# Kernel optimization log

Measured on AMD Instinct MI355X. Metric: run time of the kernel, lower is better.

## Reference

```python
import jax, jax.numpy as jnp
import numpy as np

N, E, IN, H, O, ED = 20000, 100000, 167, 4, 256, 10
HID = H * O  # 1024
BN_EPS = 1e-5


def _bn(x, g, b):
    # BatchNorm1d in training mode: batch statistics over nodes
    mu = x.mean(0)
    var = x.var(0)
    return (x - mu) * jax.lax.rsqrt(var + BN_EPS) * g + b


def _gat(x, src, dst, ef, Wg, We, attn, at, cb, heads, out):
    # modified_GAT: multi-head attention with edge features + time scalar
    n = x.shape[0]
    h = (x @ Wg).reshape(n, heads, out)                 # [N,H,O]
    e = (ef[:, 1:] @ We).reshape(-1, heads, out)        # [E,H,O] edge-feature proj
    t = ef[:, 0]                                        # [E] time feature
    # node-level attention scores (avoids materializing [E,H,O] twice)
    s_src = jnp.einsum('nhd,hd->nh', h, attn[0])
    s_dst = jnp.einsum('nhd,hd->nh', h, attn[1])
    s_e = jnp.einsum('ehd,hd->eh', e, attn[2])
    logits = jax.nn.leaky_relu(s_src[src] + s_dst[dst] + s_e + t[:, None] * at, 0.2)  # [E,H]
    # attention normalization: softmax over incoming edges of each dst node
    m = jax.ops.segment_max(logits, dst, num_segments=n)
    m = jnp.where(jnp.isfinite(m), m, 0.0)
    p = jnp.exp(logits - m[dst])
    denom = jax.ops.segment_sum(p, dst, num_segments=n)
    w = p / (denom[dst] + 1e-16)                        # [E,H]
    msg = w[:, :, None] * (h[src] + e)                  # [E,H,O]
    agg = jax.ops.segment_sum(msg, dst, num_segments=n) # [N,H,O]
    return agg.reshape(n, heads * out) + cb


def setup_inputs() -> dict:
    key = jax.random.key(0)
    ks = iter(jax.random.split(key, 64))

    def nrm(shape, s):
        return jax.random.normal(next(ks), shape, dtype=jnp.float32) * np.float32(s)

    d = {}
    d['x'] = jax.random.normal(next(ks), (N, IN), dtype=jnp.float32)
    d['edge_index'] = jax.random.randint(next(ks), (2, E), 0, N)
    d['edge_attr'] = jax.random.uniform(next(ks), (E, ED + 2), dtype=jnp.float32)
    conv_dims = [(IN, H, O), (HID, H, O), (HID, 1, 2)]
    for i, (fin, hh, oo) in enumerate(conv_dims, 1):
        d[f'Wg{i}'] = nrm((fin, hh * oo), 1.0 / np.sqrt(fin))
        d[f'We{i}'] = nrm((ED, hh * oo), 1.0 / np.sqrt(ED))
        d[f'attn{i}'] = nrm((3, hh, oo), 0.1)
        d[f'at{i}'] = nrm((hh,), 0.1)
        d[f'cb{i}'] = jnp.zeros((hh * oo,), jnp.float32)
    lin_dims = [(IN, HID), (HID, HID), (HID, 2)]
    bn_dims = [IN, HID, HID]
    for i, (fin, fo) in enumerate(lin_dims, 1):
        d[f'lw{i}'] = nrm((fin, fo), 1.0 / np.sqrt(fin))
        d[f'lb{i}'] = jnp.zeros((fo,), jnp.float32)
        d[f'g{i}'] = jnp.ones((bn_dims[i - 1],), jnp.float32)
        d[f'b{i}'] = jnp.zeros((bn_dims[i - 1],), jnp.float32)
    return d


def reference(x, edge_index, edge_attr,
              Wg1, We1, attn1, at1, cb1, lw1, lb1, g1, b1,
              Wg2, We2, attn2, at2, cb2, lw2, lb2, g2, b2,
              Wg3, We3, attn3, at3, cb3, lw3, lb3, g3, b3):
    src, dst = edge_index[0], edge_index[1]
    ef = edge_attr[:, :-1]  # drop edge class column
    h = _bn(x, g1, b1)
    h = jax.nn.relu(h @ lw1 + lb1 + _gat(h, src, dst, ef, Wg1, We1, attn1, at1, cb1, H, O))
    h = _bn(h, g2, b2)
    h = jax.nn.relu(h @ lw2 + lb2 + _gat(h, src, dst, ef, Wg2, We2, attn2, at2, cb2, H, O))
    h = _bn(h, g3, b3)
    h = jax.nn.relu(h @ lw3 + lb3 + _gat(h, src, dst, ef, Wg3, We3, attn3, at3, cb3, 1, 2))
    return h
```

## Files before the change

### kernel.cpp

```cpp
#include <hip/hip_runtime.h>
#include <math.h>

#define NN 20000
#define EE 100000
#define FIN 167
#define KP1 192
#define HID 1024
#define OO 256
#define NB 8

typedef unsigned short u16;
typedef short bf16x8 __attribute__((ext_vector_type(8)));
typedef short s16x4  __attribute__((ext_vector_type(4)));
typedef float f32x4  __attribute__((ext_vector_type(4)));

__device__ __forceinline__ float bf(u16 u){ return __uint_as_float(((unsigned)u)<<16); }
__device__ __forceinline__ u16 fb(float v){
  unsigned u = __float_as_uint(v);
  return (u16)((u + 0x7FFFu + ((u>>16)&1u)) >> 16);
}
__device__ __forceinline__ float ldv(const float* p, long i){ return p[i]; }
__device__ __forceinline__ float ldv(const u16*   p, long i){ return bf(p[i]); }

__global__ void k_count(const int* __restrict__ ei, int* __restrict__ counts){
  int e = blockIdx.x*256 + threadIdx.x;
  if (e < EE) atomicAdd(&counts[ei[EE+e]], 1);
}

__global__ __launch_bounds__(256) void k_scanA(const int* __restrict__ counts,
                                               int* __restrict__ iptr, int* __restrict__ bsum){
  __shared__ int sd[256];
  int b = blockIdx.x, tid = threadIdx.x;
  int i = b*256 + tid;
  int v = (i<NN)? counts[i] : 0;
  sd[tid]=v; __syncthreads();
  for (int off=1; off<256; off<<=1){
    int t = (tid>=off)? sd[tid-off] : 0;
    __syncthreads();
    sd[tid] += t;
    __syncthreads();
  }
  if (i<NN) iptr[i] = sd[tid]-v;
  if (tid==255) bsum[b]=sd[255];
}
__global__ __launch_bounds__(128) void k_scanB(const int* __restrict__ bsum,
                                               int* __restrict__ boff, int* __restrict__ iptrN,
                                               int nb){
  __shared__ int sd[128];
  int tid=threadIdx.x;
  int v=(tid<nb)? bsum[tid]:0;
  sd[tid]=v; __syncthreads();
  for (int off=1; off<128; off<<=1){
    int t=(tid>=off)?sd[tid-off]:0;
    __syncthreads();
    sd[tid]+=t;
    __syncthreads();
  }
  if (tid<nb) boff[tid]=sd[tid]-v;
  if (tid==127) *iptrN = sd[127];
}
__global__ void k_scanC(const int* __restrict__ boff, int* __restrict__ iptr){
  int i = blockIdx.x*256+threadIdx.x;
  if (i<NN) iptr[i] += boff[blockIdx.x];
}

__global__ void k_fill(const int* __restrict__ ei, const int* __restrict__ iptr,
                       int* __restrict__ cursor, int* __restrict__ eid){
  int e = blockIdx.x*256 + threadIdx.x;
  if (e < EE){
    int d = ei[EE+e];
    int pos = atomicAdd(&cursor[d],1);
    eid[iptr[d]+pos] = e;
  }
}

template<typename T>
__global__ void k_bnstats(const T* __restrict__ X, float* __restrict__ sums, int F){
  int f = blockIdx.y*256 + threadIdx.x;
  if (f >= F) return;
  int r0 = blockIdx.x*100, r1 = r0+100;
  float s=0.f, s2=0.f;
  for (int r=r0;r<r1;r++){ float v = ldv(X,(long)r*F+f); s += v; s2 += v*v; }
  atomicAdd(&sums[f], s);
  atomicAdd(&sums[F+f], s2);
}

__global__ __launch_bounds__(256) void k_bnstats8(const u16* __restrict__ X, float* __restrict__ part){
  int tid = threadIdx.x;
  int f8 = (tid & 127)*8;
  int r0 = blockIdx.x*79, r1 = min(NN, r0+79);
  float s[8]={0,0,0,0,0,0,0,0}, s2[8]={0,0,0,0,0,0,0,0};
  for (int r=r0 + (tid>>7); r<r1; r+=2){
    bf16x8 v = *(const bf16x8*)(X + (long)r*HID + f8);
    #pragma unroll
    for (int j=0;j<8;j++){ float x=bf((u16)v[j]); s[j]+=x; s2[j]+=x*x; }
  }
  __shared__ float red[256][8];
  float* pb = part + (long)blockIdx.x*2048;
  #pragma unroll
  for (int j=0;j<8;j++) red[tid][j]=s[j];
  __syncthreads();
  if (tid<128){
    #pragma unroll
    for (int j=0;j<8;j++) pb[f8+j] = red[tid][j]+red[tid+128][j];
  }
  __syncthreads();
  #pragma unroll
  for (int j=0;j<8;j++) red[tid][j]=s2[j];
  __syncthreads();
  if (tid<128){
    #pragma unroll
    for (int j=0;j<8;j++) pb[1024+f8+j] = red[tid][j]+red[tid+128][j];
  }
}

__global__ __launch_bounds__(256) void k_pred(const float* __restrict__ part, float* __restrict__ sums){
  int idx = blockIdx.x*256 + threadIdx.x;
  float s = 0.f;
  #pragma unroll 8
  for (int b=0;b<256;b++) s += part[(long)b*2048 + idx];
  sums[idx] = s;
}

__global__ void k_bnfin(const float* __restrict__ sums, const float* __restrict__ g,
                        const float* __restrict__ b, float* __restrict__ scale,
                        float* __restrict__ shift, int F){
  int f = blockIdx.x*256 + threadIdx.x;
  if (f >= F) return;
  float mu  = sums[f]   * (1.f/NN);
  float var = sums[F+f] * (1.f/NN) - mu*mu;
  float sc  = rsqrtf(var + 1e-5f) * g[f];
  scale[f] = sc;
  shift[f] = b[f] - mu*sc;
}

__global__ __launch_bounds__(256) void k_foldT(const float* __restrict__ Wg, const float* __restrict__ Wl,
                        const float* __restrict__ scale,
                        u16* __restrict__ Wt, int K, int Kp){
  __shared__ float t[32][33];
  int k0 = blockIdx.x*32, c0 = blockIdx.y*32;
  int tx = threadIdx.x & 31, ty = threadIdx.x >> 5;
  bool second = (c0 >= HID);
  const float* W = second ? Wl : Wg;
  int cc0 = second ? c0 - HID : c0;
  #pragma unroll
  for (int i=0;i<4;i++){
    int k = k0 + ty + i*8;
    t[ty+i*8][tx] = (k < K) ? W[(long)k*HID + cc0 + tx] * scale[k] : 0.f;
  }
  __syncthreads();
  #pragma unroll
  for (int i=0;i<4;i++){
    int c = c0 + ty + i*8;
    Wt[(long)c*Kp + k0 + tx] = fb(t[tx][ty+i*8]);
  }
}

__global__ void k_cinit(const float* __restrict__ lb, float* __restrict__ cst){
  int c = blockIdx.x*256 + threadIdx.x;
  if (c < 2*HID) cst[c] = (c >= HID) ? lb[c-HID] : 0.f;
}

__global__ __launch_bounds__(256) void k_const(const float* __restrict__ Wg, const float* __restrict__ Wl,
                        const float* __restrict__ shift, float* __restrict__ cst, int K){
  int tx = threadIdx.x & 63, ty = threadIdx.x >> 6;
  int c = blockIdx.x*64 + tx;
  bool second = c >= HID;
  const float* W = second ? Wl : Wg;
  int cc = second ? c-HID : c;
  int k0 = blockIdx.y*128;
  int k1 = min(K, k0+128);
  float s = 0.f;
  for (int k=k0+ty; k<k1; k+=4) s += shift[k]*W[(long)k*HID+cc];
  __shared__ float red[256];
  red[threadIdx.x] = s;
  __syncthreads();
  if (ty == 0){
    float tot = red[tx] + red[tx+64] + red[tx+128] + red[tx+192];
    atomicAdd(&cst[c], tot);
  }
}

__global__ void k_cast(const float* __restrict__ x, u16* __restrict__ xb){
  long idx = (long)blockIdx.x*256 + threadIdx.x;
  if (idx >= (long)NN*KP1) return;
  int n = (int)(idx / KP1), k = (int)(idx % KP1);
  xb[idx] = (k<FIN)? fb(x[(long)n*FIN+k]) : (u16)0;
}

__global__ void k_we16(const float* __restrict__ We, u16* __restrict__ We16){
  int i = blockIdx.x*256 + threadIdx.x;
  if (i < 10*HID) We16[i] = fb(We[i]);
}

#define MF(a_,b_,c_) __builtin_amdgcn_mfma_f32_16x16x32_bf16(a_,b_,c_,0,0,0)
#define FENCE asm volatile("" ::: "memory")
#define BAR do { FENCE; __builtin_amdgcn_s_barrier(); FENCE; } while(0)

__global__ __launch_bounds__(512,2) void k_gemm(const u16* __restrict__ A, int K,
                     const u16* __restrict__ Wt, const float* __restrict__ cst,
                     u16* __restrict__ Chg, u16* __restrict__ Clin){
  __shared__ u16 lds[3][12288];
  int b = blockIdx.x;
  int wg = (b & 7)*158 + (b >> 3);
  int row0 = (wg >> 4)*256, col0 = (wg & 15)*128;
  int tid = threadIdx.x;
  int wave = tid >> 6, lane = tid & 63, quad = lane >> 4, lo = lane & 15;
  int wm = wave >> 1, wn = wave & 1;
  const u16* Apt[2];
  #pragma unroll
  for (int i=0;i<2;i++){
    int s = i*512 + tid, srow = s>>2;
    int gr = row0 + srow; if (gr >= NN) gr = NN-1;
    Apt[i] = A + (long)gr*K + (((s&3)^((srow>>1)&3))*8);
  }
  int brow = tid>>2;
  const u16* Bpt = Wt + (long)(col0 + brow)*K + ((((tid&3)^((brow>>1)&3)))*8);
  const char* ldsc = (const char*)&lds[0][0];
  int axor = (lo>>1) & 3;
  int aoff = (wm*64 + lo)*64 + ((quad^axor)*16);
  int boff = 16384 + (wn*64 + lo)*64 + ((quad^axor)*16);
  int NT = K >> 5;
  f32x4 acc[4][4] = {};
  {
    u16* d0 = (u16*)&lds[0][0];
    u16* d1 = (u16*)&lds[1][0];
    __builtin_amdgcn_global_load_lds(Apt[0],      d0 +         tid*8, 16, 0, 0);
    __builtin_amdgcn_global_load_lds(Apt[1],      d0 + 4096 +  tid*8, 16, 0, 0);
    __builtin_amdgcn_global_load_lds(Bpt,         d0 + 8192 +  tid*8, 16, 0, 0);
    __builtin_amdgcn_global_load_lds(Apt[0] + 32, d1 +         tid*8, 16, 0, 0);
    __builtin_amdgcn_global_load_lds(Apt[1] + 32, d1 + 4096 +  tid*8, 16, 0, 0);
    __builtin_amdgcn_global_load_lds(Bpt    + 32, d1 + 8192 +  tid*8, 16, 0, 0);
    asm volatile("s_waitcnt vmcnt(3)" ::: "memory");
    BAR;
  }
  int cb = 0;
  for (int t=0; t<NT; t++){
    const char* Lb = ldsc + cb*24576;
    bf16x8 af[4], bfr[4];
    #pragma unroll
    for (int i=0;i<4;i++) af[i]  = *(const bf16x8*)(Lb + aoff + i*1024);
    #pragma unroll
    for (int n=0;n<4;n++) bfr[n] = *(const bf16x8*)(Lb + boff + n*1024);
    int nx2 = (t+2 < NT);
    if (nx2){
      int sb = cb+2; if (sb>=3) sb-=3;
      u16* Sd = (u16*)&lds[0][0] + sb*12288;
      int ko = (t+2) << 5;
      __builtin_amdgcn_global_load_lds(Apt[0] + ko, Sd +         tid*8, 16, 0, 0);
      __builtin_amdgcn_global_load_lds(Apt[1] + ko, Sd + 4096 +  tid*8, 16, 0, 0);
      __builtin_amdgcn_global_load_lds(Bpt    + ko, Sd + 8192 +  tid*8, 16, 0, 0);
    }
    __builtin_amdgcn_s_setprio(1);
    #pragma unroll
    for (int i=0;i<4;i++)
      #pragma unroll
      for (int n=0;n<4;n++)
        acc[i][n] = MF(af[i], bfr[n], acc[i][n]);
    __builtin_amdgcn_s_setprio(0);
    if (t+1 < NT){
      if (nx2) asm volatile("s_waitcnt vmcnt(3)" ::: "memory");
      else     asm volatile("s_waitcnt vmcnt(0)" ::: "memory");
      BAR;
    }
    cb++; if (cb>=3) cb=0;
  }
  #pragma unroll
  for (int i=0;i<4;i++){
    #pragma unroll
    for (int n=0;n<4;n++){
      int col = col0 + wn*64 + n*16 + lo;
      float cs = cst[col];
      #pragma unroll
      for (int r=0;r<4;r++){
        int row = row0 + wm*64 + i*16 + quad*4 + r;
        if (row < NN){
          u16 o = fb(acc[i][n][r] + cs);
          if (col < HID) Chg[(long)row*HID + col] = o;
          else           Clin[(long)row*HID + col - HID] = o;
        }
      }
    }
  }
}
#undef MF
#undef BAR
#undef FENCE

__global__ __launch_bounds__(256) void k_sdot(const u16* __restrict__ hg, const float* __restrict__ attn,
                       float* __restrict__ ssrc, float* __restrict__ sdst){
  int unit = blockIdx.x*4 + (threadIdx.x >> 6);
  if (unit >= NN*4) return;
  int lane = threadIdx.x & 63;
  int n = unit >> 2, h = unit & 3;
  const u16* hp = hg + (long)n*HID + h*OO + lane*4;
  s16x4 v = *(const s16x4*)hp;
  float4 x0 = *(const float4*)(attn + h*OO + lane*4);
  float4 x1 = *(const float4*)(attn + HID + h*OO + lane*4);
  float f0 = bf((u16)v.x), f1 = bf((u16)v.y), f2 = bf((u16)v.z), f3 = bf((u16)v.w);
  float ss = f0*x0.x + f1*x0.y + f2*x0.z + f3*x0.w;
  float sd = f0*x1.x + f1*x1.y + f2*x1.z + f3*x1.w;
  #pragma unroll
  for (int off=32; off>0; off>>=1){
    ss += __shfl_down(ss, off);
    sd += __shfl_down(sd, off);
  }
  if (lane==0){ ssrc[unit]=ss; sdst[unit]=sd; }
}

__global__ void k_q(const float* __restrict__ We, const float* __restrict__ attn,
                    float* __restrict__ q){
  int t = threadIdx.x;
  if (t >= 40) return;
  int k = t >> 2, h = t & 3;
  float s = 0.f;
  for (int d=0; d<OO; d++) s += We[(long)k*HID + h*OO + d] * attn[2*HID + h*OO + d];
  q[k*4+h] = s;
}

__global__ void k_logits(const int* __restrict__ ei, const float* __restrict__ ea,
                         const float* __restrict__ q, const float* __restrict__ at,
                         const float* __restrict__ ssrc, const float* __restrict__ sdst,
                         float* __restrict__ L){
  int e = blockIdx.x*256 + threadIdx.x;
  if (e >= EE) return;
  int s = ei[e], dd = ei[EE+e];
  float4 a0 = *(const float4*)(ea + (long)e*12);
  float4 a1 = *(const float4*)(ea + (long)e*12 + 4);
  float4 a2 = *(const float4*)(ea + (long)e*12 + 8);
  float t = a0.x;
  float cc[10] = {a0.y,a0.z,a0.w, a1.x,a1.y,a1.z,a1.w, a2.x,a2.y,a2.z};
  float4 ss = *(const float4*)(ssrc + (long)s*4);
  float4 sd = *(const float4*)(sdst + (long)dd*4);
  float sv[4] = {ss.x+sd.x, ss.y+sd.y, ss.z+sd.z, ss.w+sd.w};
  float4 out;
  #pragma unroll
  for (int h=0;h<4;h++){
    float se = 0.f;
    #pragma unroll
    for (int k=0;k<10;k++) se += cc[k]*q[k*4+h];
    float v = sv[h] + se + t*at[h];
    ((float*)&out)[h] = (v>0.f)? v : 0.2f*v;
  }
  *(float4*)(L + (long)e*4) = out;
}

__global__ void k_mden(const int* __restrict__ iptr, const int* __restrict__ eid,
                       const float* __restrict__ ea, float* __restrict__ L,
                       float* __restrict__ cw){
  int n = blockIdx.x*256 + threadIdx.x;
  if (n >= NN) return;
  int b = iptr[n], e1 = iptr[n+1];
  float m0=-INFINITY, m1=-INFINITY, m2=-INFINITY, m3=-INFINITY;
  for (int i=b;i<e1;i++){
    float4 l = *(const float4*)(L + (long)eid[i]*4);
    m0=fmaxf(m0,l.x); m1=fmaxf(m1,l.y); m2=fmaxf(m2,l.z); m3=fmaxf(m3,l.w);
  }
  if (b==e1){ m0=m1=m2=m3=0.f; }
  float s0=0.f,s1=0.f,s2=0.f,s3=0.f;
  for (int i=b;i<e1;i++){
    float4 l = *(const float4*)(L + (long)eid[i]*4);
    s0+=expf(l.x-m0); s1+=expf(l.y-m1); s2+=expf(l.z-m2); s3+=expf(l.w-m3);
  }
  float d0=1.f/(s0+1e-16f), d1=1.f/(s1+1e-16f), d2=1.f/(s2+1e-16f), d3=1.f/(s3+1e-16f);
  float c[4][10] = {};
  for (int i=b;i<e1;i++){
    int e = eid[i];
    float4 l = *(const float4*)(L + (long)e*4);
    float4 w = { expf(l.x-m0)*d0, expf(l.y-m1)*d1, expf(l.z-m2)*d2, expf(l.w-m3)*d3 };
    *(float4*)(L + (long)e*4) = w;
    float4 a0 = *(const float4*)(ea + (long)e*12);
    float4 a1 = *(const float4*)(ea + (long)e*12 + 4);
    float4 a2 = *(const float4*)(ea + (long)e*12 + 8);
    float cc[10] = {a0.y,a0.z,a0.w, a1.x,a1.y,a1.z,a1.w, a2.x,a2.y,a2.z};
    #pragma unroll
    for (int k=0;k<10;k++){
      c[0][k] += w.x*cc[k]; c[1][k] += w.y*cc[k];
      c[2][k] += w.z*cc[k]; c[3][k] += w.w*cc[k];
    }
  }
  float* cp = cw + (long)n*40;
  #pragma unroll
  for (int h=0;h<4;h++)
    #pragma unroll
    for (int k=0;k<10;k++) cp[h*10+k] = c[h][k];
}

__global__ __launch_bounds__(256) void k_gath(
    const u16* __restrict__ hg, const int* __restrict__ ei,
    const int* __restrict__ iptr, const int* __restrict__ eid,
    const float* __restrict__ L,
    const float* __restrict__ cw,
    const u16* __restrict__ We16, const float* __restrict__ cb,
    u16* __restrict__ lio)
{
  __shared__ u16  sWe[10*HID];
  __shared__ float scb[HID];
  int tid = threadIdx.x;
  for (int i=tid;i<10*HID;i+=256) sWe[i] = We16[i];
  for (int i=tid;i<HID;i+=256) scb[i] = cb[i];
  __syncthreads();
  int h = tid >> 6;
  int f0 = tid*4;
  int d0 = blockIdx.x*NB, dend = min(NN, d0+NB);
  for (int d=d0; d<dend; d++){
    s16x4 a0 = *(const s16x4*)(lio + (long)d*HID + f0);
    float acc0=bf((u16)a0.x), acc1=bf((u16)a0.y), acc2=bf((u16)a0.z), acc3=bf((u16)a0.w);
    int b0 = iptr[d], en = iptr[d+1];
    float wN = 0.f; s16x4 vN = {};
    if (b0 < en){
      int e = eid[b0], s_ = ei[e];
      wN = L[(long)e*4 + h];
      vN = *(const s16x4*)(hg + (long)s_*HID + f0);
    }
    for (int i=b0;i<en;i++){
      float w = wN; s16x4 v = vN;
      if (i+1 < en){
        int e2 = eid[i+1], s2 = ei[e2];
        wN = L[(long)e2*4 + h];
        vN = *(const s16x4*)(hg + (long)s2*HID + f0);
      }
      acc0 += w*bf((u16)v.x); acc1 += w*bf((u16)v.y);
      acc2 += w*bf((u16)v.z); acc3 += w*bf((u16)v.w);
    }
    const float* cp = cw + (long)d*40 + h*10;
    float ew0=0.f, ew1=0.f, ew2=0.f, ew3=0.f;
    #pragma unroll
    for (int k=0;k<10;k++){
      float c = cp[k];
      s16x4 wv = *(const s16x4*)(sWe + k*HID + f0);
      ew0 += c*bf((u16)wv.x); ew1 += c*bf((u16)wv.y);
      ew2 += c*bf((u16)wv.z); ew3 += c*bf((u16)wv.w);
    }
    acc0 += ew0; acc1 += ew1; acc2 += ew2; acc3 += ew3;
    u16 o[4];
    o[0] = fb(fmaxf(acc0 + scb[f0  ], 0.f));
    o[1] = fb(fmaxf(acc1 + scb[f0+1], 0.f));
    o[2] = fb(fmaxf(acc2 + scb[f0+2], 0.f));
    o[3] = fb(fmaxf(acc3 + scb[f0+3], 0.f));
    *(s16x4*)(lio + (long)d*HID + f0) = *(const s16x4*)o;
  }
}

__global__ void k_c4init(const float* __restrict__ lb, float* __restrict__ c4){
  if (threadIdx.x==0 && blockIdx.x==0){ c4[0]=0.f; c4[1]=0.f; c4[2]=lb[0]; c4[3]=lb[1]; }
}

__global__ __launch_bounds__(256) void k_fold3(const float* __restrict__ Wg, const float* __restrict__ lw,
                        const float* __restrict__ scale, const float* __restrict__ shift,
                        float* __restrict__ W4, float* __restrict__ c4){
  int k = blockIdx.x*256 + threadIdx.x;
  float sc = scale[k], sh = shift[k];
  float w0=Wg[k*2], w1=Wg[k*2+1], l0=lw[k*2], l1=lw[k*2+1];
  float4 o = {w0*sc, w1*sc, l0*sc, l1*sc};
  *(float4*)(W4 + (long)k*4) = o;
  __shared__ float red[256][4];
  int tid = threadIdx.x;
  red[tid][0]=sh*w0; red[tid][1]=sh*w1; red[tid][2]=sh*l0; red[tid][3]=sh*l1;
  __syncthreads();
  for (int o2=128;o2>0;o2>>=1){
    if (tid<o2){
      #pragma unroll
      for (int j=0;j<4;j++) red[tid][j]+=red[tid+o2][j];
    }
    __syncthreads();
  }
  if (tid==0){
    #pragma unroll
    for (int j=0;j<4;j++) atomicAdd(&c4[j], red[0][j]);
  }
}

__global__ __launch_bounds__(256) void k_n3(const u16* __restrict__ in,
    const float* __restrict__ W4, const float* __restrict__ c4,
    const float* __restrict__ attn,
    float* __restrict__ hg3, float* __restrict__ lin3,
    float* __restrict__ ssrc, float* __restrict__ sdst)
{
  __shared__ float sW[HID*4];
  __shared__ float sx[4][HID];
  int tid = threadIdx.x;
  int n0 = blockIdx.x*4;
  for (int i=tid; i<HID; i+=256) *(float4*)&sW[i*4] = *(const float4*)(W4 + (long)i*4);
  for (int idx=tid; idx<512; idx+=256){
    int rr = idx>>7, ch = idx&127;
    bf16x8 v = *(const bf16x8*)(in + (long)(n0+rr)*HID + ch*8);
    #pragma unroll
    for (int j=0;j<8;j++) sx[rr][ch*8+j] = bf((u16)v[j]);
  }
  __syncthreads();
  int w = tid>>6, lane = tid&63;
  float p0=0.f,p1=0.f,p2=0.f,p3=0.f;
  #pragma unroll
  for (int g=0; g<16; g++){
    int k = g*64 + lane;
    float x = sx[w][k];
    float4 wv = *(const float4*)&sW[k*4];
    p0 += x*wv.x; p1 += x*wv.y; p2 += x*wv.z; p3 += x*wv.w;
  }
  #pragma unroll
  for (int off=32; off>0; off>>=1){
    p0 += __shfl_down(p0, off);
    p1 += __shfl_down(p1, off);
    p2 += __shfl_down(p2, off);
    p3 += __shfl_down(p3, off);
  }
  if (lane==0){
    int n = n0 + w;
    float r0=p0+c4[0], r1=p1+c4[1], r2=p2+c4[2], r3=p3+c4[3];
    hg3[n*2]=r0; hg3[n*2+1]=r1;
    lin3[n*2]=r2; lin3[n*2+1]=r3;
    ssrc[n]=r0*attn[0]+r1*attn[1];
    sdst[n]=r0*attn[2]+r1*attn[3];
  }
}

__global__ void k_logits3(const int* __restrict__ ei, const float* __restrict__ ea,
                          const float* __restrict__ We, const float* __restrict__ attn,
                          const float* __restrict__ at, const float* __restrict__ ssrc,
                          const float* __restrict__ sdst, float* __restrict__ L){
  int e = blockIdx.x*256 + threadIdx.x;
  if (e >= EE) return;
  int s = ei[e], d = ei[EE+e];
  float e0=0.f, e1=0.f;
  #pragma unroll
  for (int k=0;k<10;k++){
    float c = ea[e*12+1+k];
    e0 += c*We[k*2]; e1 += c*We[k*2+1];
  }
  float se = e0*attn[4] + e1*attn[5];
  float v = ssrc[s] + sdst[d] + se + ea[e*12]*at[0];
  L[e] = (v>0.f)? v : 0.2f*v;
}

__global__ void k_mden3(const int* __restrict__ iptr, const int* __restrict__ eid,
                        const float* __restrict__ ea, float* __restrict__ L,
                        float* __restrict__ cw){
  int n = blockIdx.x*256 + threadIdx.x;
  if (n >= NN) return;
  int b = iptr[n], e1 = iptr[n+1];
  float mx = -INFINITY;
  for (int i=b;i<e1;i++) mx = fmaxf(mx, L[eid[i]]);
  if (b == e1) mx = 0.f;
  float s = 0.f;
  for (int i=b;i<e1;i++) s += expf(L[eid[i]] - mx);
  float dv = 1.f/(s+1e-16f);
  float c[10] = {0.f,0.f,0.f,0.f,0.f,0.f,0.f,0.f,0.f,0.f};
  for (int i=b;i<e1;i++){
    int e = eid[i];
    float w = expf(L[e]-mx)*dv;
    L[e] = w;
    #pragma unroll
    for (int k=0;k<10;k++) c[k] += w*ea[e*12+1+k];
  }
  float* cp = cw + (long)n*10;
  #pragma unroll
  for (int k=0;k<10;k++) cp[k] = c[k];
}

__global__ void k_gather3(const int* __restrict__ ei,
                          const int* __restrict__ iptr, const int* __restrict__ eid,
                          const float* __restrict__ L,
                          const float* __restrict__ cw,
                          const float* __restrict__ hg3,
                          const float* __restrict__ We, const float* __restrict__ lin3,
                          const float* __restrict__ cb, float* __restrict__ out){
  int n = blockIdx.x*256 + threadIdx.x;
  if (n >= NN) return;
  int b = iptr[n], en = iptr[n+1];
  const float* cp = cw + (long)n*10;
  float e0f=0.f, e1f=0.f;
  #pragma unroll
  for (int k=0;k<10;k++){ e0f += cp[k]*We[k*2]; e1f += cp[k]*We[k*2+1]; }
  float a0=0.f, a1=0.f;
  for (int i=b;i<en;i++){
    int e = eid[i], s_ = ei[e];
    float w = L[e];
    a0 += w*hg3[s_*2];
    a1 += w*hg3[s_*2+1];
  }
  out[n*2]   = fmaxf(lin3[n*2]  +a0+e0f+cb[0], 0.f);
  out[n*2+1] = fmaxf(lin3[n*2+1]+a1+e1f+cb[1], 0.f);
}

extern "C" void kernel_launch(void* const* d_in, const int* in_sizes, int n_in,
                              void* d_out, int out_size, void* d_ws, size_t ws_size,
                              hipStream_t stream){
  const int* ei = (const int*)d_in[1];

  long long sz[64];
  {
    const long long* s64 = (const long long*)(const void*)in_sizes;
    bool is64 = (n_in >= 2) && (in_sizes[0] == 3340000) && (in_sizes[1] == 0)
                && (s64[1] == 200000);
    for (int i=0;i<n_in && i<64;i++) sz[i] = is64 ? s64[i] : (long long)in_sizes[i];
  }

  int IWg[3], IWe[3], IAttn[3], IAt[3], ICb[3], ILw[3], ILb[3], IG[3], IB[3];
  if (n_in > 8 && sz[8] == (long long)HID*HID){
    for (int l=0;l<3;l++){
      IWg[l]=3+l*5; IWe[l]=4+l*5; IAttn[l]=5+l*5; IAt[l]=6+l*5; ICb[l]=7+l*5;
      ILw[l]=18+l*4; ILb[l]=19+l*4; IG[l]=20+l*4; IB[l]=21+l*4;
    }
  } else {
    int idx=3;
    for (int l=0;l<3;l++){
      IWg[l]=idx++; IWe[l]=idx++; IAttn[l]=idx++; IAt[l]=idx++; ICb[l]=idx++;
      ILw[l]=idx++; ILb[l]=idx++; IG[l]=idx++; IB[l]=idx++;
    }
  }
  #define FP(i) ((const float*)d_in[(i)])

  char* ws = (char*)d_ws;
  size_t off = 0;
  auto alloc = [&](size_t bytes)->void*{ void* p = ws + off; off += (bytes + 255) & ~(size_t)255; return p; };
  auto G = [](long n){ return (int)((n+255)/256); };

  u16*   buf0 = (u16*)  alloc((size_t)NN*HID*2);
  u16*   bufA = (u16*)  alloc((size_t)NN*HID*2);
  u16*   bufB = (u16*)  alloc((size_t)NN*HID*2);
  u16*   xbf  = (u16*)  alloc((size_t)NN*KP1*2);
  u16*   Wt   = (u16*)  alloc((size_t)2*HID*HID*2);
  u16*   We16 = (u16*)  alloc((size_t)10*HID*2);
  float* cst  = (float*)alloc(2*HID*4);
  float* L    = (float*)alloc((size_t)EE*4*4);
  float* ssrc = (float*)alloc((size_t)NN*4*4);
  float* sdst = (float*)alloc((size_t)NN*4*4);
  int*   iptr = (int*)  alloc((size_t)(NN+4)*4);
  int*   cnts = (int*)  alloc((size_t)NN*4);
  int*   eid  = (int*)  alloc((size_t)EE*4);
  int*   bsum = (int*)  alloc(256*4);
  int*   boff = (int*)  alloc(256*4);
  float* stats= (float*)alloc(2*HID*4);
  float* scale= (float*)alloc(HID*4);
  float* shift= (float*)alloc(HID*4);
  float* qbuf = (float*)alloc(64*4);
  float* hg3  = (float*)alloc((size_t)NN*2*4);
  float* lin3 = (float*)alloc((size_t)NN*2*4);
  float* cw   = (float*)alloc((size_t)NN*40*4);
  float* W4   = (float*)alloc((size_t)HID*4*4);
  float* c4   = (float*)alloc(4*4);
  float* part = (float*)alloc((size_t)256*2048*4);

  int nsb = G(NN);
  hipMemsetAsync(cnts, 0, NN*sizeof(int), stream);
  k_count<<<G(EE),256,0,stream>>>(ei, cnts);
  k_scanA<<<nsb,256,0,stream>>>(cnts, iptr, bsum);
  k_scanB<<<1,128,0,stream>>>(bsum, boff, iptr+NN, nsb);
  k_scanC<<<nsb,256,0,stream>>>(boff, iptr);
  hipMemsetAsync(cnts, 0, NN*sizeof(int), stream);
  k_fill<<<G(EE),256,0,stream>>>(ei, iptr, cnts, eid);

  int gg = 1264;
  int gsd = (NN*4+3)/4;

  {
    hipMemsetAsync(stats, 0, 2*FIN*sizeof(float), stream);
    dim3 bg(200, 1);
    k_bnstats<float><<<bg,256,0,stream>>>(FP(0), stats, FIN);
    k_bnfin<<<1,256,0,stream>>>(stats, FP(IG[0]), FP(IB[0]), scale, shift, FIN);
    k_cast<<<G((long)NN*KP1),256,0,stream>>>(FP(0), xbf);
    dim3 ft(KP1/32, 64);
    k_foldT<<<ft,256,0,stream>>>(FP(IWg[0]), FP(ILw[0]), scale, Wt, FIN, KP1);
    k_cinit<<<8,256,0,stream>>>(FP(ILb[0]), cst);
    dim3 cg(32, (FIN+127)/128);
    k_const<<<cg,256,0,stream>>>(FP(IWg[0]), FP(ILw[0]), shift, cst, FIN);
    k_we16<<<40,256,0,stream>>>(FP(IWe[0]), We16);
    k_gemm<<<gg,512,0,stream>>>(xbf, KP1, Wt, cst, buf0, bufA);
    k_sdot<<<gsd,256,0,stream>>>(buf0, FP(IAttn[0]), ssrc, sdst);
    k_q<<<1,64,0,stream>>>(FP(IWe[0]), FP(IAttn[0]), qbuf);
    k_logits<<<G(EE),256,0,stream>>>(ei, FP(2), qbuf, FP(IAt[0]), ssrc, sdst, L);
    k_mden<<<G(NN),256,0,stream>>>(iptr, eid, FP(2), L, cw);
    k_gath<<<(NN+NB-1)/NB,256,0,stream>>>(buf0, ei, iptr, eid, L, cw,
                                          We16, FP(ICb[0]), bufA);
  }
  {
    k_bnstats8<<<256,256,0,stream>>>(bufA, part);
    k_pred<<<8,256,0,stream>>>(part, stats);
    k_bnfin<<<4,256,0,stream>>>(stats, FP(IG[1]), FP(IB[1]), scale, shift, HID);
    dim3 ft(HID/32, 64);
    k_foldT<<<ft,256,0,stream>>>(FP(IWg[1]), FP(ILw[1]), scale, Wt, HID, HID);
    k_cinit<<<8,256,0,stream>>>(FP(ILb[1]), cst);
    dim3 cg(32, HID/128);
    k_const<<<cg,256,0,stream>>>(FP(IWg[1]), FP(ILw[1]), shift, cst, HID);
    k_we16<<<40,256,0,stream>>>(FP(IWe[1]), We16);
    k_gemm<<<gg,512,0,stream>>>(bufA, HID, Wt, cst, buf0, bufB);
    k_sdot<<<gsd,256,0,stream>>>(buf0, FP(IAttn[1]), ssrc, sdst);
    k_q<<<1,64,0,stream>>>(FP(IWe[1]), FP(IAttn[1]), qbuf);
    k_logits<<<G(EE),256,0,stream>>>(ei, FP(2), qbuf, FP(IAt[1]), ssrc, sdst, L);
    k_mden<<<G(NN),256,0,stream>>>(iptr, eid, FP(2), L, cw);
    k_gath<<<(NN+NB-1)/NB,256,0,stream>>>(buf0, ei, iptr, eid, L, cw,
                                          We16, FP(ICb[1]), bufB);
  }

  k_bnstats8<<<256,256,0,stream>>>(bufB, part);
  k_pred<<<8,256,0,stream>>>(part, stats);
  k_bnfin<<<4,256,0,stream>>>(stats, FP(IG[2]), FP(IB[2]), scale, shift, HID);
  k_c4init<<<1,64,0,stream>>>(FP(ILb[2]), c4);
  k_fold3<<<HID/256,256,0,stream>>>(FP(IWg[2]), FP(ILw[2]), scale, shift, W4, c4);
  k_n3<<<NN/4,256,0,stream>>>(bufB, W4, c4, FP(IAttn[2]), hg3, lin3, ssrc, sdst);
  k_logits3<<<G(EE),256,0,stream>>>(ei, FP(2), FP(IWe[2]), FP(IAttn[2]), FP(IAt[2]), ssrc, sdst, L);
  k_mden3<<<G(NN),256,0,stream>>>(iptr, eid, FP(2), L, cw);
  k_gather3<<<G(NN),256,0,stream>>>(ei, iptr, eid, L, cw, hg3,
                                    FP(IWe[2]), lin3, FP(ICb[2]), (float*)d_out);
}
```

Before: 759.8 us.

## Defer softmax normalization to gather, drop extra exp pass and setprio

The softmax kernels no longer do a separate pass to sum exponentials. They store unnormalized exp weights, accumulate the sum inside the edge-feature loop, and write per-node reciprocal denominators that the gather kernels apply once after accumulation. This removes one full pass over each node's incoming edges (gathers plus exp) in the mden kernels. Those kernels also move to 128-thread blocks to spread the small per-node work over more workgroups. The GEMM's s_setprio around the MFMA block is removed, which may change how wave scheduling interleaves with loads.

```diff
diff --git a/kernel.cpp b/kernel.cpp
--- a/kernel.cpp
+++ b/kernel.cpp
@@ -251,13 +251,11 @@
       __builtin_amdgcn_global_load_lds(Apt[1] + ko, Sd + 4096 +  tid*8, 16, 0, 0);
       __builtin_amdgcn_global_load_lds(Bpt    + ko, Sd + 8192 +  tid*8, 16, 0, 0);
     }
-    __builtin_amdgcn_s_setprio(1);
     #pragma unroll
     for (int i=0;i<4;i++)
       #pragma unroll
       for (int n=0;n<4;n++)
         acc[i][n] = MF(af[i], bfr[n], acc[i][n]);
-    __builtin_amdgcn_s_setprio(0);
     if (t+1 < NT){
       if (nx2) asm volatile("s_waitcnt vmcnt(3)" ::: "memory");
       else     asm volatile("s_waitcnt vmcnt(0)" ::: "memory");
@@ -345,10 +343,10 @@
   *(float4*)(L + (long)e*4) = out;
 }
 
-__global__ void k_mden(const int* __restrict__ iptr, const int* __restrict__ eid,
+__global__ __launch_bounds__(128) void k_mden(const int* __restrict__ iptr, const int* __restrict__ eid,
                        const float* __restrict__ ea, float* __restrict__ L,
-                       float* __restrict__ cw){
-  int n = blockIdx.x*256 + threadIdx.x;
+                       float* __restrict__ cw, float* __restrict__ dv4){
+  int n = blockIdx.x*128 + threadIdx.x;
   if (n >= NN) return;
   int b = iptr[n], e1 = iptr[n+1];
   float m0=-INFINITY, m1=-INFINITY, m2=-INFINITY, m3=-INFINITY;
@@ -358,32 +356,34 @@
   }
   if (b==e1){ m0=m1=m2=m3=0.f; }
   float s0=0.f,s1=0.f,s2=0.f,s3=0.f;
-  for (int i=b;i<e1;i++){
-    float4 l = *(const float4*)(L + (long)eid[i]*4);
-    s0+=expf(l.x-m0); s1+=expf(l.y-m1); s2+=expf(l.z-m2); s3+=expf(l.w-m3);
-  }
-  float d0=1.f/(s0+1e-16f), d1=1.f/(s1+1e-16f), d2=1.f/(s2+1e-16f), d3=1.f/(s3+1e-16f);
   float c[4][10] = {};
   for (int i=b;i<e1;i++){
     int e = eid[i];
     float4 l = *(const float4*)(L + (long)e*4);
-    float4 w = { expf(l.x-m0)*d0, expf(l.y-m1)*d1, expf(l.z-m2)*d2, expf(l.w-m3)*d3 };
-    *(float4*)(L + (long)e*4) = w;
+    float4 p = { expf(l.x-m0), expf(l.y-m1), expf(l.z-m2), expf(l.w-m3) };
+    *(float4*)(L + (long)e*4) = p;
+    s0+=p.x; s1+=p.y; s2+=p.z; s3+=p.w;
     float4 a0 = *(const float4*)(ea + (long)e*12);
     float4 a1 = *(const float4*)(ea + (long)e*12 + 4);
     float4 a2 = *(const float4*)(ea + (long)e*12 + 8);
     float cc[10] = {a0.y,a0.z,a0.w, a1.x,a1.y,a1.z,a1.w, a2.x,a2.y,a2.z};
     #pragma unroll
     for (int k=0;k<10;k++){
-      c[0][k] += w.x*cc[k]; c[1][k] += w.y*cc[k];
-      c[2][k] += w.z*cc[k]; c[3][k] += w.w*cc[k];
-    }
-  }
+      c[0][k] += p.x*cc[k]; c[1][k] += p.y*cc[k];
+      c[2][k] += p.z*cc[k]; c[3][k] += p.w*cc[k];
+    }
+  }
+  float d0=1.f/(s0+1e-16f), d1=1.f/(s1+1e-16f), d2=1.f/(s2+1e-16f), d3=1.f/(s3+1e-16f);
   float* cp = cw + (long)n*40;
   #pragma unroll
-  for (int h=0;h<4;h++)
-    #pragma unroll
-    for (int k=0;k<10;k++) cp[h*10+k] = c[h][k];
+  for (int k=0;k<10;k++){
+    cp[k]    = c[0][k]*d0;
+    cp[10+k] = c[1][k]*d1;
+    cp[20+k] = c[2][k]*d2;
+    cp[30+k] = c[3][k]*d3;
+  }
+  float4 dv = {d0,d1,d2,d3};
+  *(float4*)(dv4 + (long)n*4) = dv;
 }
 
 __global__ __launch_bounds__(256) void k_gath(
@@ -391,6 +391,7 @@
     const int* __restrict__ iptr, const int* __restrict__ eid,
     const float* __restrict__ L,
     const float* __restrict__ cw,
+    const float* __restrict__ dv4,
     const u16* __restrict__ We16, const float* __restrict__ cb,
     u16* __restrict__ lio)
 {
@@ -406,6 +407,8 @@
   for (int d=d0; d<dend; d++){
     s16x4 a0 = *(const s16x4*)(lio + (long)d*HID + f0);
     float acc0=bf((u16)a0.x), acc1=bf((u16)a0.y), acc2=bf((u16)a0.z), acc3=bf((u16)a0.w);
+    float gt0=0.f, gt1=0.f, gt2=0.f, gt3=0.f;
+    float dv = dv4[(long)d*4 + h];
     int b0 = iptr[d], en = iptr[d+1];
     float wN = 0.f; s16x4 vN = {};
     if (b0 < en){
@@ -420,9 +423,10 @@
         wN = L[(long)e2*4 + h];
         vN = *(const s16x4*)(hg + (long)s2*HID + f0);
       }
-      acc0 += w*bf((u16)v.x); acc1 += w*bf((u16)v.y);
-      acc2 += w*bf((u16)v.z); acc3 += w*bf((u16)v.w);
-    }
+      gt0 += w*bf((u16)v.x); gt1 += w*bf((u16)v.y);
+      gt2 += w*bf((u16)v.z); gt3 += w*bf((u16)v.w);
+    }
+    acc0 += dv*gt0; acc1 += dv*gt1; acc2 += dv*gt2; acc3 += dv*gt3;
     const float* cp = cw + (long)d*40 + h*10;
     float ew0=0.f, ew1=0.f, ew2=0.f, ew3=0.f;
     #pragma unroll
@@ -533,39 +537,41 @@
   L[e] = (v>0.f)? v : 0.2f*v;
 }
 
-__global__ void k_mden3(const int* __restrict__ iptr, const int* __restrict__ eid,
+__global__ __launch_bounds__(128) void k_mden3(const int* __restrict__ iptr, const int* __restrict__ eid,
                         const float* __restrict__ ea, float* __restrict__ L,
-                        float* __restrict__ cw){
-  int n = blockIdx.x*256 + threadIdx.x;
+                        float* __restrict__ cw, float* __restrict__ dvn){
+  int n = blockIdx.x*128 + threadIdx.x;
   if (n >= NN) return;
   int b = iptr[n], e1 = iptr[n+1];
   float mx = -INFINITY;
   for (int i=b;i<e1;i++) mx = fmaxf(mx, L[eid[i]]);
   if (b == e1) mx = 0.f;
   float s = 0.f;
-  for (int i=b;i<e1;i++) s += expf(L[eid[i]] - mx);
-  float dv = 1.f/(s+1e-16f);
   float c[10] = {0.f,0.f,0.f,0.f,0.f,0.f,0.f,0.f,0.f,0.f};
   for (int i=b;i<e1;i++){
     int e = eid[i];
-    float w = expf(L[e]-mx)*dv;
-    L[e] = w;
-    #pragma unroll
-    for (int k=0;k<10;k++) c[k] += w*ea[e*12+1+k];
-  }
+    float p = expf(L[e]-mx);
+    L[e] = p;
+    s += p;
+    #pragma unroll
+    for (int k=0;k<10;k++) c[k] += p*ea[e*12+1+k];
+  }
+  float dv = 1.f/(s+1e-16f);
   float* cp = cw + (long)n*10;
   #pragma unroll
-  for (int k=0;k<10;k++) cp[k] = c[k];
-}
-
-__global__ void k_gather3(const int* __restrict__ ei,
+  for (int k=0;k<10;k++) cp[k] = c[k]*dv;
+  dvn[n] = dv;
+}
+
+__global__ __launch_bounds__(128) void k_gather3(const int* __restrict__ ei,
                           const int* __restrict__ iptr, const int* __restrict__ eid,
                           const float* __restrict__ L,
                           const float* __restrict__ cw,
+                          const float* __restrict__ dvn,
                           const float* __restrict__ hg3,
                           const float* __restrict__ We, const float* __restrict__ lin3,
                           const float* __restrict__ cb, float* __restrict__ out){
-  int n = blockIdx.x*256 + threadIdx.x;
+  int n = blockIdx.x*128 + threadIdx.x;
   if (n >= NN) return;
   int b = iptr[n], en = iptr[n+1];
   const float* cp = cw + (long)n*10;
@@ -579,8 +585,9 @@
     a0 += w*hg3[s_*2];
     a1 += w*hg3[s_*2+1];
   }
-  out[n*2]   = fmaxf(lin3[n*2]  +a0+e0f+cb[0], 0.f);
-  out[n*2+1] = fmaxf(lin3[n*2+1]+a1+e1f+cb[1], 0.f);
+  float dv = dvn[n];
+  out[n*2]   = fmaxf(lin3[n*2]  +dv*a0+e0f+cb[0], 0.f);
+  out[n*2+1] = fmaxf(lin3[n*2+1]+dv*a1+e1f+cb[1], 0.f);
 }
 
 extern "C" void kernel_launch(void* const* d_in, const int* in_sizes, int n_in,
@@ -626,6 +633,7 @@
   float* L    = (float*)alloc((size_t)EE*4*4);
   float* ssrc = (float*)alloc((size_t)NN*4*4);
   float* sdst = (float*)alloc((size_t)NN*4*4);
+  float* dv4  = (float*)alloc((size_t)NN*4*4);
   int*   iptr = (int*)  alloc((size_t)(NN+4)*4);
   int*   cnts = (int*)  alloc((size_t)NN*4);
   int*   eid  = (int*)  alloc((size_t)EE*4);
@@ -653,6 +661,7 @@
 
   int gg = 1264;
   int gsd = (NN*4+3)/4;
+  int gnd = (NN+127)/128;
 
   {
     hipMemsetAsync(stats, 0, 2*FIN*sizeof(float), stream);
@@ -670,8 +679,8 @@
     k_sdot<<<gsd,256,0,stream>>>(buf0, FP(IAttn[0]), ssrc, sdst);
     k_q<<<1,64,0,stream>>>(FP(IWe[0]), FP(IAttn[0]), qbuf);
     k_logits<<<G(EE),256,0,stream>>>(ei, FP(2), qbuf, FP(IAt[0]), ssrc, sdst, L);
-    k_mden<<<G(NN),256,0,stream>>>(iptr, eid, FP(2), L, cw);
-    k_gath<<<(NN+NB-1)/NB,256,0,stream>>>(buf0, ei, iptr, eid, L, cw,
+    k_mden<<<gnd,128,0,stream>>>(iptr, eid, FP(2), L, cw, dv4);
+    k_gath<<<(NN+NB-1)/NB,256,0,stream>>>(buf0, ei, iptr, eid, L, cw, dv4,
                                           We16, FP(ICb[0]), bufA);
   }
   {
@@ -688,8 +697,8 @@
     k_sdot<<<gsd,256,0,stream>>>(buf0, FP(IAttn[1]), ssrc, sdst);
     k_q<<<1,64,0,stream>>>(FP(IWe[1]), FP(IAttn[1]), qbuf);
     k_logits<<<G(EE),256,0,stream>>>(ei, FP(2), qbuf, FP(IAt[1]), ssrc, sdst, L);
-    k_mden<<<G(NN),256,0,stream>>>(iptr, eid, FP(2), L, cw);
-    k_gath<<<(NN+NB-1)/NB,256,0,stream>>>(buf0, ei, iptr, eid, L, cw,
+    k_mden<<<gnd,128,0,stream>>>(iptr, eid, FP(2), L, cw, dv4);
+    k_gath<<<(NN+NB-1)/NB,256,0,stream>>>(buf0, ei, iptr, eid, L, cw, dv4,
                                           We16, FP(ICb[1]), bufB);
   }
 
@@ -700,7 +709,7 @@
   k_fold3<<<HID/256,256,0,stream>>>(FP(IWg[2]), FP(ILw[2]), scale, shift, W4, c4);
   k_n3<<<NN/4,256,0,stream>>>(bufB, W4, c4, FP(IAttn[2]), hg3, lin3, ssrc, sdst);
   k_logits3<<<G(EE),256,0,stream>>>(ei, FP(2), FP(IWe[2]), FP(IAttn[2]), FP(IAt[2]), ssrc, sdst, L);
-  k_mden3<<<G(NN),256,0,stream>>>(iptr, eid, FP(2), L, cw);
-  k_gather3<<<G(NN),256,0,stream>>>(ei, iptr, eid, L, cw, hg3,
-                                    FP(IWe[2]), lin3, FP(ICb[2]), (float*)d_out);
-}
+  k_mden3<<<gnd,128,0,stream>>>(iptr, eid, FP(2), L, cw, dv4);
+  k_gather3<<<gnd,128,0,stream>>>(ei, iptr, eid, L, cw, dv4, hg3,
+                                  FP(IWe[2]), lin3, FP(ICb[2]), (float*)d_out);
+}
```

New measurement: 732.3 us. 1.04x faster.
